# Optimization experiments

Hardware: AMD Instinct MI355X
Metric: run time of the kernel (lower is better)

The kernel has to match this reference:

```python
import jax, jax.numpy as jnp
import numpy as np

SIGNAL_LEN = 2048
N_WAVELETS = 32
TWO_PI = 2.0 * np.pi


def _encoder(x, W1, b1, W2, b2, W3, b3, W4, b4):
    B = x.shape[0]
    h = x.reshape(B, -1)                      # (B, 4096)
    h = jax.nn.relu(h @ W1.T + b1)            # (B, 1024)
    h = jax.nn.relu(h @ W2.T + b2)            # (B, 512)
    h = jax.nn.relu(h @ W3.T + b3)            # (B, 256)
    return h @ W4.T + b4                      # (B, n_wavelets*5)


def _synthesize(params):
    # params: (B, N_WAVELETS, 5)
    A = params[..., 0]                                    # (B, N)
    t0 = jax.nn.sigmoid(params[..., 1]) * SIGNAL_LEN      # (B, N)
    f = jax.nn.sigmoid(params[..., 2]) * 0.5              # (B, N)
    sigma = jax.nn.sigmoid(params[..., 3]) * 200.0 + 2.0  # (B, N)
    phi = params[..., 4]                                  # (B, N)

    t = jnp.arange(SIGNAL_LEN, dtype=params.dtype)        # (T,)
    dt = t[None, None, :] - t0[..., None]                 # (B, N, T)
    g = (A[..., None]
         * jnp.exp(-(dt * dt) / (2.0 * sigma[..., None] ** 2))
         * jnp.cos(TWO_PI * f[..., None] * dt + phi[..., None]))  # (B, N, T)
    sig = jnp.sum(g, axis=1)                              # (B, T)
    # both channels receive the identical wavelet sum (as in the torch code)
    return jnp.stack([sig, sig], axis=1)                  # (B, 2, T)


def setup_inputs() -> dict:
    key = jax.random.key(0)
    ks = jax.random.split(key, 9)
    B = 4096
    def w(k, shape, fan_in):
        return jax.random.normal(k, shape, dtype=jnp.float32) / np.sqrt(fan_in)
    return {
        "x": jax.random.normal(ks[0], (B, 2, SIGNAL_LEN), dtype=jnp.float32),
        "W1": w(ks[1], (1024, 4096), 4096), "b1": jnp.zeros((1024,), jnp.float32),
        "W2": w(ks[2], (512, 1024), 1024),  "b2": jnp.zeros((512,), jnp.float32),
        "W3": w(ks[3], (256, 512), 512),    "b3": jnp.zeros((256,), jnp.float32),
        "W4": w(ks[4], (N_WAVELETS * 5, 256), 256), "b4": jnp.zeros((N_WAVELETS * 5,), jnp.float32),
    }


def reference(x, W1, b1, W2, b2, W3, b3, W4, b4):
    B = x.shape[0]
    params = _encoder(x, W1, b1, W2, b2, W3, b3, W4, b4).reshape(B, N_WAVELETS, 5)
    return _synthesize(params)  # (B, 2, SIGNAL_LEN)
```

## Files before the change

### kernel.cpp

```cpp
#include <hip/hip_runtime.h>


#define SIGNAL_LEN 2048
#define NWAV 32

typedef _Float16 f16x8 __attribute__((ext_vector_type(8)));
typedef _Float16 f16x4 __attribute__((ext_vector_type(4)));
typedef float    f32x4 __attribute__((ext_vector_type(4)));

__device__ __forceinline__ void load16_lds(const _Float16* g, _Float16* l) {
  __builtin_amdgcn_global_load_lds((const __attribute__((address_space(1))) void*)g,
                                   (__attribute__((address_space(3))) void*)l,
                                   16, 0, 0);
}

struct HL { _Float16 h, l; };
__device__ __forceinline__ HL split_one(float a) {
  HL r;
  r.h = (_Float16)a;
  r.l = (_Float16)((a - (float)r.h) * 4096.0f);
  return r;
}

__global__ void split_x(const float4* __restrict__ src, f16x4* __restrict__ dh,
                        f16x4* __restrict__ dl) {
  int i = blockIdx.x * 256 + threadIdx.x;
  float4 v = src[i];
  float a[4] = {v.x, v.y, v.z, v.w};
  f16x4 h, l;
#pragma unroll
  for (int j = 0; j < 4; j++) {
    HL r = split_one(a[j]);
    h[j] = r.h;
    l[j] = r.l;
  }
  dh[i] = h;
  dl[i] = l;
}

__global__ void split_weights(const float* __restrict__ W1, const float* __restrict__ W2,
                              const float* __restrict__ W3, const float* __restrict__ W4,
                              const float* __restrict__ b4,
                              f16x4* __restrict__ W1h, f16x4* __restrict__ W1l,
                              f16x4* __restrict__ W2h, f16x4* __restrict__ W2l,
                              f16x4* __restrict__ W3h, f16x4* __restrict__ W3l,
                              f16x4* __restrict__ W4h, f16x4* __restrict__ W4l,
                              float* __restrict__ b4p) {
  const int blk = blockIdx.x;
  const int tid = threadIdx.x;
  if (blk < 4736) {
    const float4* src;
    f16x4 *dh, *dl;
    int i;
    if (blk < 4096) {
      src = (const float4*)W1; dh = W1h; dl = W1l; i = blk * 256 + tid;
    } else if (blk < 4608) {
      src = (const float4*)W2; dh = W2h; dl = W2l; i = (blk - 4096) * 256 + tid;
    } else {
      src = (const float4*)W3; dh = W3h; dl = W3l; i = (blk - 4608) * 256 + tid;
    }
    float4 v = src[i];
    float a[4] = {v.x * 256.0f, v.y * 256.0f, v.z * 256.0f, v.w * 256.0f};
    f16x4 h, l;
#pragma unroll
    for (int j = 0; j < 4; j++) {
      HL r = split_one(a[j]);
      h[j] = r.h;
      l[j] = r.l;
    }
    dh[i] = h;
    dl[i] = l;
  } else if (blk < 4800) {
    int i = (blk - 4736) * 256 + tid;
    int i4 = i << 2;
    int row = i4 >> 8;
    f16x4 h, l;
#pragma unroll
    for (int j = 0; j < 4; j++) {
      float a = (row < 160) ? W4[i4 + j] * 256.0f : 0.0f;
      HL r = split_one(a);
      h[j] = r.h;
      l[j] = r.l;
    }
    W4h[i] = h;
    W4l[i] = l;
  } else {
    b4p[tid] = (tid < 160) ? b4[tid] : 0.0f;
  }
}

template <int TM, int TN, int N, int K, bool RELU, bool SPLIT_OUT>
__global__ void __launch_bounds__(256, 2)
gemm_db(const _Float16* __restrict__ Ah, const _Float16* __restrict__ Al,
        const _Float16* __restrict__ Bh, const _Float16* __restrict__ Bl,
        const float* __restrict__ bias,
        _Float16* __restrict__ Ch, _Float16* __restrict__ Cl,
        float* __restrict__ Cf) {
  constexpr int AM = TM / 32;
  constexpr int BN = TN / 32;
  constexpr int AU = TM / 8;
  constexpr int TU = (TM + TN) / 8;
  constexpr int UPW = TU / 4;
  constexpr int NK = K / 32;

  __shared__ __align__(16) _Float16 s[2][(TM + TN) * 64];

  const int tid = threadIdx.x;
  const int lane = tid & 63;
  const int w = tid >> 6;
  const int wm = w >> 1, wn = w & 1;
  const int m0 = blockIdx.y * TM;
  const int n0 = blockIdx.x * TN;

  const int srow = lane >> 2;
  const int sk8 = (((lane & 3) - (lane >> 3)) & 3) * 8;

  const _Float16* gb[UPW];
  int lo[UPW];
#pragma unroll
  for (int i = 0; i < UPW; ++i) {
    const int u = w * UPW + i;
    if (u < AU) {
      const int g = u >> 1, hl = u & 1;
      gb[i] = (hl ? Al : Ah) + (size_t)(m0 + g * 16 + srow) * K + sk8;
    } else {
      const int ub = u - AU;
      const int g = ub >> 1, hl = ub & 1;
      gb[i] = (hl ? Bl : Bh) + (size_t)(n0 + g * 16 + srow) * K + sk8;
    }
    lo[i] = u * 512;
  }

  const int fr = lane & 15;
  const int fq = lane >> 4;
  const int fslot8 = (4 * fr + ((fq + (fr >> 1)) & 3)) * 8;

  f32x4 acc1[AM][BN], acc2[AM][BN];
#pragma unroll
  for (int i = 0; i < AM; i++)
#pragma unroll
    for (int j = 0; j < BN; j++) {
      acc1[i][j] = 0.0f;
      acc2[i][j] = 0.0f;
    }

#pragma unroll
  for (int i = 0; i < UPW; ++i) load16_lds(gb[i], &s[0][lo[i]]);

  for (int kt = 0; kt < NK; ++kt) {
    const int cur = kt & 1;
    __syncthreads();

    if (kt + 1 < NK) {
      const int kofs = (kt + 1) * 32;
#pragma unroll
      for (int i = 0; i < UPW; ++i) load16_lds(gb[i] + kofs, &s[cur ^ 1][lo[i]]);
    }

    f16x8 fAh[AM], fAl[AM], fBh[BN], fBl[BN];
#pragma unroll
    for (int im = 0; im < AM; ++im) {
      const int g = wm * AM + im;
      fAh[im] = *(const f16x8*)(&s[cur][(g * 2 + 0) * 512 + fslot8]);
      fAl[im] = *(const f16x8*)(&s[cur][(g * 2 + 1) * 512 + fslot8]);
    }
#pragma unroll
    for (int in = 0; in < BN; ++in) {
      const int g = wn * BN + in;
      fBh[in] = *(const f16x8*)(&s[cur][TM * 64 + (g * 2 + 0) * 512 + fslot8]);
      fBl[in] = *(const f16x8*)(&s[cur][TM * 64 + (g * 2 + 1) * 512 + fslot8]);
    }
#pragma unroll
    for (int im = 0; im < AM; ++im) {
#pragma unroll
      for (int in = 0; in < BN; ++in) {
        acc1[im][in] = __builtin_amdgcn_mfma_f32_16x16x32_f16(fAh[im], fBh[in], acc1[im][in], 0, 0, 0);
        acc2[im][in] = __builtin_amdgcn_mfma_f32_16x16x32_f16(fAh[im], fBl[in], acc2[im][in], 0, 0, 0);
        acc2[im][in] = __builtin_amdgcn_mfma_f32_16x16x32_f16(fAl[im], fBh[in], acc2[im][in], 0, 0, 0);
      }
    }
  }

  const int quad = lane >> 4;
#pragma unroll
  for (int in = 0; in < BN; ++in) {
    const int n = n0 + wn * (TN / 2) + in * 16 + fr;
    const float bv = bias[n];
#pragma unroll
    for (int im = 0; im < AM; ++im) {
#pragma unroll
      for (int r = 0; r < 4; ++r) {
        const int m = m0 + wm * (TM / 2) + im * 16 + quad * 4 + r;
        float c = (acc1[im][in][r] + acc2[im][in][r] * (1.0f / 4096.0f)) * (1.0f / 256.0f) + bv;
        if (RELU) c = fmaxf(c, 0.0f);
        const size_t off = (size_t)m * N + n;
        if (SPLIT_OUT) {
          HL rr = split_one(c);
          Ch[off] = rr.h;
          Cl[off] = rr.l;
        } else {
          Cf[off] = c;
        }
      }
    }
  }
}

__global__ void __launch_bounds__(256)
synth(const float* __restrict__ P, float* __restrict__ out) {
  __shared__ float sA[NWAV], sT0[NWAV], sF[NWAV], sC[NWAV], sPh[NWAV], sSg[NWAV];
  const int b = blockIdx.x;
  const int tid = threadIdx.x;
  if (tid < NWAV) {
    const float* q = P + (size_t)b * 256 + tid * 5;
    const float L2E = 1.44269504088896340736f;
    float A = q[0], p1 = q[1], p2 = q[2], p3 = q[3], p4 = q[4];
    float s1 = 1.0f / (1.0f + exp2f(-p1 * L2E));
    float s2 = 1.0f / (1.0f + exp2f(-p2 * L2E));
    float s3 = 1.0f / (1.0f + exp2f(-p3 * L2E));
    float sg = s3 * 200.0f + 2.0f;
    sA[tid] = A;
    sT0[tid] = s1 * 2048.0f;
    sF[tid] = s2 * 0.5f;
    sC[tid] = -L2E / (2.0f * sg * sg);
    sPh[tid] = p4 * 0.15915494309189535f;
    sSg[tid] = sg;
  }
  __syncthreads();

  const float t0f = (float)(tid * 8);
  const int wlo = (tid & ~63) * 8;
  float acc[8];
#pragma unroll
  for (int i = 0; i < 8; i++) acc[i] = 0.0f;

  for (int wv = 0; wv < NWAV; wv++) {
    const float t0 = sT0[wv], sg = sSg[wv];
    if (t0 + 5.0f * sg < (float)wlo || t0 - 5.0f * sg > (float)(wlo + 511)) continue;
    const float A = sA[wv], fr = sF[wv], cn = sC[wv], ph = sPh[wv];
#pragma unroll
    for (int i = 0; i < 8; i++) {
      float dt = (t0f + (float)i) - t0;
      float e = exp2f(dt * dt * cn);
      float r = fr * dt + ph;
      r -= floorf(r);
      float cs = __builtin_amdgcn_cosf(r);
      acc[i] += A * e * cs;
    }
  }

  float* o = out + (size_t)b * (2 * SIGNAL_LEN) + tid * 8;
  float4 v0 = make_float4(acc[0], acc[1], acc[2], acc[3]);
  float4 v1 = make_float4(acc[4], acc[5], acc[6], acc[7]);
  *(float4*)(o) = v0;
  *(float4*)(o + 4) = v1;
  *(float4*)(o + SIGNAL_LEN) = v0;
  *(float4*)(o + SIGNAL_LEN + 4) = v1;
}

extern "C" void kernel_launch(void* const* d_in, const int* in_sizes, int n_in,
                              void* d_out, int out_size, void* d_ws, size_t ws_size,
                              hipStream_t stream) {
  (void)in_sizes; (void)n_in; (void)out_size; (void)ws_size;
  const float* X  = (const float*)d_in[0];
  const float* W1 = (const float*)d_in[1];
  const float* b1 = (const float*)d_in[2];
  const float* W2 = (const float*)d_in[3];
  const float* b2 = (const float*)d_in[4];
  const float* W3 = (const float*)d_in[5];
  const float* b3 = (const float*)d_in[6];
  const float* W4 = (const float*)d_in[7];
  const float* b4 = (const float*)d_in[8];
  float* out = (float*)d_out;

  char* p = (char*)d_ws;
  auto take = [&](size_t bytes) -> char* {
    char* r = p;
    p += (bytes + 255) & ~(size_t)255;
    return r;
  };
  _Float16* Xh  = (_Float16*)take((size_t)4096 * 4096 * 2);
  _Float16* Xl  = (_Float16*)take((size_t)4096 * 4096 * 2);
  _Float16* W1h = (_Float16*)take((size_t)1024 * 4096 * 2);
  _Float16* W1l = (_Float16*)take((size_t)1024 * 4096 * 2);
  _Float16* H1h = (_Float16*)take((size_t)4096 * 1024 * 2);
  _Float16* H1l = (_Float16*)take((size_t)4096 * 1024 * 2);
  _Float16* W2h = (_Float16*)take((size_t)512 * 1024 * 2);
  _Float16* W2l = (_Float16*)take((size_t)512 * 1024 * 2);
  _Float16* H2h = (_Float16*)take((size_t)4096 * 512 * 2);
  _Float16* H2l = (_Float16*)take((size_t)4096 * 512 * 2);
  _Float16* W3h = (_Float16*)take((size_t)256 * 512 * 2);
  _Float16* W3l = (_Float16*)take((size_t)256 * 512 * 2);
  _Float16* H3h = (_Float16*)take((size_t)4096 * 256 * 2);
  _Float16* H3l = (_Float16*)take((size_t)4096 * 256 * 2);
  _Float16* W4h = (_Float16*)take((size_t)256 * 256 * 2);
  _Float16* W4l = (_Float16*)take((size_t)256 * 256 * 2);
  float*    b4p = (float*)take(256 * 4);
  float*    Pp  = (float*)take((size_t)4096 * 256 * 4);

  split_x<<<16384, 256, 0, stream>>>((const float4*)X, (f16x4*)Xh, (f16x4*)Xl);
  split_weights<<<4801, 256, 0, stream>>>(W1, W2, W3, W4, b4,
                                          (f16x4*)W1h, (f16x4*)W1l, (f16x4*)W2h, (f16x4*)W2l,
                                          (f16x4*)W3h, (f16x4*)W3l, (f16x4*)W4h, (f16x4*)W4l, b4p);

  gemm_db<128, 128, 1024, 4096, true, true><<<dim3(8, 32), 256, 0, stream>>>(
      Xh, Xl, W1h, W1l, b1, H1h, H1l, nullptr);
  gemm_db<64, 128, 512, 1024, true, true><<<dim3(4, 64), 256, 0, stream>>>(
      H1h, H1l, W2h, W2l, b2, H2h, H2l, nullptr);
  gemm_db<64, 64, 256, 512, true, true><<<dim3(4, 64), 256, 0, stream>>>(
      H2h, H2l, W3h, W3l, b3, H3h, H3l, nullptr);
  gemm_db<64, 64, 256, 256, false, false><<<dim3(4, 64), 256, 0, stream>>>(
      H3h, H3l, W4h, W4l, b4p, nullptr, nullptr, Pp);

  synth<<<4096, 256, 0, stream>>>(Pp, out);
}
```

Before: 405.4 us.

## Split GEMM K dimension in two and add a separate combine epilogue kernel

Each encoder GEMM now runs with a two-way split over K via a grid z-dimension. Each split writes fp32 partial sums to a scratch buffer, and a new combine kernel adds them, applies scale, bias and ReLU, and re-splits the result into fp16 hi/lo pairs. The aim is to double the block count so more of the GPU's compute units are busy, since the first GEMM had only 256 blocks. The cost is extra fp32 partial-sum traffic through global memory and four additional kernel launches.

Measured after the change: 437.4 us. 1.08x slower.

```diff
diff --git a/kernel.cpp b/kernel.cpp
--- a/kernel.cpp
+++ b/kernel.cpp
@@ -89,19 +89,17 @@
   }
 }
 
-template <int TM, int TN, int N, int K, bool RELU, bool SPLIT_OUT>
+template <int TM, int TN, int N, int K, int KSPLIT>
 __global__ void __launch_bounds__(256, 2)
 gemm_db(const _Float16* __restrict__ Ah, const _Float16* __restrict__ Al,
         const _Float16* __restrict__ Bh, const _Float16* __restrict__ Bl,
-        const float* __restrict__ bias,
-        _Float16* __restrict__ Ch, _Float16* __restrict__ Cl,
-        float* __restrict__ Cf) {
+        float* __restrict__ Cp) {
   constexpr int AM = TM / 32;
   constexpr int BN = TN / 32;
   constexpr int AU = TM / 8;
   constexpr int TU = (TM + TN) / 8;
   constexpr int UPW = TU / 4;
-  constexpr int NK = K / 32;
+  constexpr int NK = K / KSPLIT / 32;
 
   __shared__ __align__(16) _Float16 s[2][(TM + TN) * 64];
 
@@ -111,6 +109,7 @@
   const int wm = w >> 1, wn = w & 1;
   const int m0 = blockIdx.y * TM;
   const int n0 = blockIdx.x * TN;
+  const int kb = blockIdx.z * (K / KSPLIT);
 
   const int srow = lane >> 2;
   const int sk8 = (((lane & 3) - (lane >> 3)) & 3) * 8;
@@ -122,11 +121,11 @@
     const int u = w * UPW + i;
     if (u < AU) {
       const int g = u >> 1, hl = u & 1;
-      gb[i] = (hl ? Al : Ah) + (size_t)(m0 + g * 16 + srow) * K + sk8;
+      gb[i] = (hl ? Al : Ah) + (size_t)(m0 + g * 16 + srow) * K + kb + sk8;
     } else {
       const int ub = u - AU;
       const int g = ub >> 1, hl = ub & 1;
-      gb[i] = (hl ? Bl : Bh) + (size_t)(n0 + g * 16 + srow) * K + sk8;
+      gb[i] = (hl ? Bl : Bh) + (size_t)(n0 + g * 16 + srow) * K + kb + sk8;
     }
     lo[i] = u * 512;
   }
@@ -182,27 +181,50 @@
   }
 
   const int quad = lane >> 4;
+  float* Cz = Cp + (size_t)blockIdx.z * ((size_t)gridDim.y * TM) * N;
 #pragma unroll
   for (int in = 0; in < BN; ++in) {
     const int n = n0 + wn * (TN / 2) + in * 16 + fr;
-    const float bv = bias[n];
 #pragma unroll
     for (int im = 0; im < AM; ++im) {
 #pragma unroll
       for (int r = 0; r < 4; ++r) {
         const int m = m0 + wm * (TM / 2) + im * 16 + quad * 4 + r;
-        float c = (acc1[im][in][r] + acc2[im][in][r] * (1.0f / 4096.0f)) * (1.0f / 256.0f) + bv;
-        if (RELU) c = fmaxf(c, 0.0f);
-        const size_t off = (size_t)m * N + n;
-        if (SPLIT_OUT) {
-          HL rr = split_one(c);
-          Ch[off] = rr.h;
-          Cl[off] = rr.l;
-        } else {
-          Cf[off] = c;
-        }
+        Cz[(size_t)m * N + n] = acc1[im][in][r] + acc2[im][in][r] * (1.0f / 4096.0f);
       }
     }
+  }
+}
+
+template <bool RELU, bool SPLIT_OUT>
+__global__ void __launch_bounds__(256)
+combine(const float* __restrict__ Cp, const float* __restrict__ bias, int N,
+        size_t halfN, _Float16* __restrict__ Ch, _Float16* __restrict__ Cl,
+        float* __restrict__ Cf) {
+  const size_t i4 = ((size_t)blockIdx.x * 256 + threadIdx.x) * 4;
+  float4 p0 = *(const float4*)(Cp + i4);
+  float4 p1 = *(const float4*)(Cp + halfN + i4);
+  float4 bv = *(const float4*)(bias + (i4 % (size_t)N));
+  float c[4] = {(p0.x + p1.x) * (1.0f / 256.0f) + bv.x,
+                (p0.y + p1.y) * (1.0f / 256.0f) + bv.y,
+                (p0.z + p1.z) * (1.0f / 256.0f) + bv.z,
+                (p0.w + p1.w) * (1.0f / 256.0f) + bv.w};
+  if (RELU) {
+#pragma unroll
+    for (int j = 0; j < 4; j++) c[j] = fmaxf(c[j], 0.0f);
+  }
+  if (SPLIT_OUT) {
+    f16x4 h, l;
+#pragma unroll
+    for (int j = 0; j < 4; j++) {
+      HL r = split_one(c[j]);
+      h[j] = r.h;
+      l[j] = r.l;
+    }
+    *(f16x4*)(Ch + i4) = h;
+    *(f16x4*)(Cl + i4) = l;
+  } else {
+    *(float4*)(Cf + i4) = make_float4(c[0], c[1], c[2], c[3]);
   }
 }
 
@@ -297,20 +319,32 @@
   _Float16* W4l = (_Float16*)take((size_t)256 * 256 * 2);
   float*    b4p = (float*)take(256 * 4);
   float*    Pp  = (float*)take((size_t)4096 * 256 * 4);
+  float*    Cp  = (float*)take((size_t)2 * 4096 * 1024 * 4);
 
   split_x<<<16384, 256, 0, stream>>>((const float4*)X, (f16x4*)Xh, (f16x4*)Xl);
   split_weights<<<4801, 256, 0, stream>>>(W1, W2, W3, W4, b4,
                                           (f16x4*)W1h, (f16x4*)W1l, (f16x4*)W2h, (f16x4*)W2l,
                                           (f16x4*)W3h, (f16x4*)W3l, (f16x4*)W4h, (f16x4*)W4l, b4p);
 
-  gemm_db<128, 128, 1024, 4096, true, true><<<dim3(8, 32), 256, 0, stream>>>(
-      Xh, Xl, W1h, W1l, b1, H1h, H1l, nullptr);
-  gemm_db<64, 128, 512, 1024, true, true><<<dim3(4, 64), 256, 0, stream>>>(
-      H1h, H1l, W2h, W2l, b2, H2h, H2l, nullptr);
-  gemm_db<64, 64, 256, 512, true, true><<<dim3(4, 64), 256, 0, stream>>>(
-      H2h, H2l, W3h, W3l, b3, H3h, H3l, nullptr);
-  gemm_db<64, 64, 256, 256, false, false><<<dim3(4, 64), 256, 0, stream>>>(
-      H3h, H3l, W4h, W4l, b4p, nullptr, nullptr, Pp);
+  gemm_db<128, 128, 1024, 4096, 2><<<dim3(8, 32, 2), 256, 0, stream>>>(
+      Xh, Xl, W1h, W1l, Cp);
+  combine<true, true><<<4096, 256, 0, stream>>>(
+      Cp, b1, 1024, (size_t)4096 * 1024, H1h, H1l, nullptr);
+
+  gemm_db<64, 128, 512, 1024, 2><<<dim3(4, 64, 2), 256, 0, stream>>>(
+      H1h, H1l, W2h, W2l, Cp);
+  combine<true, true><<<2048, 256, 0, stream>>>(
+      Cp, b2, 512, (size_t)4096 * 512, H2h, H2l, nullptr);
+
+  gemm_db<64, 64, 256, 512, 2><<<dim3(4, 64, 2), 256, 0, stream>>>(
+      H2h, H2l, W3h, W3l, Cp);
+  combine<true, true><<<1024, 256, 0, stream>>>(
+      Cp, b3, 256, (size_t)4096 * 256, H3h, H3l, nullptr);
+
+  gemm_db<64, 64, 256, 256, 2><<<dim3(4, 64, 2), 256, 0, stream>>>(
+      H3h, H3l, W4h, W4l, Cp);
+  combine<false, false><<<1024, 256, 0, stream>>>(
+      Cp, b4p, 256, (size_t)4096 * 256, nullptr, nullptr, Pp);
 
   synth<<<4096, 256, 0, stream>>>(Pp, out);
 }
```

## Split-K the first GEMM with larger tiles and a separate combine kernel

Applied to the files above, without the earlier changes.

The first layer GEMM (4096x1024x4096) changes from 128x128 tiles on a 256-block grid to 128x256 tiles split over K in two halves, still 256 blocks but with occupancy hint 1. Each half writes fp32 partial sums to a new 32 MB buffer, and a combine kernel adds them, applies bias and ReLU, and splits the result into fp16 hi/lo. The larger N tile is meant to raise operand reuse per block. The cost is an extra fp32 round-trip of the partials, one more launch, and more registers per thread.

After: 404.3 us. Within noise of the previous version (-0.3%).

```diff
diff --git a/kernel.cpp b/kernel.cpp
--- a/kernel.cpp
+++ b/kernel.cpp
@@ -91,11 +91,11 @@
 
 template <int TM, int TN, int N, int K, bool RELU, bool SPLIT_OUT>
 __global__ void __launch_bounds__(256, 2)
-gemm_db(const _Float16* __restrict__ Ah, const _Float16* __restrict__ Al,
-        const _Float16* __restrict__ Bh, const _Float16* __restrict__ Bl,
-        const float* __restrict__ bias,
-        _Float16* __restrict__ Ch, _Float16* __restrict__ Cl,
-        float* __restrict__ Cf) {
+gemm_fused(const _Float16* __restrict__ Ah, const _Float16* __restrict__ Al,
+           const _Float16* __restrict__ Bh, const _Float16* __restrict__ Bl,
+           const float* __restrict__ bias,
+           _Float16* __restrict__ Ch, _Float16* __restrict__ Cl,
+           float* __restrict__ Cf) {
   constexpr int AM = TM / 32;
   constexpr int BN = TN / 32;
   constexpr int AU = TM / 8;
@@ -204,6 +204,136 @@
       }
     }
   }
+}
+
+template <int TM, int TN, int N, int K, int KSPLIT, int MINW>
+__global__ void __launch_bounds__(256, MINW)
+gemm_part(const _Float16* __restrict__ Ah, const _Float16* __restrict__ Al,
+          const _Float16* __restrict__ Bh, const _Float16* __restrict__ Bl,
+          float* __restrict__ Cp) {
+  constexpr int AM = TM / 32;
+  constexpr int BN = TN / 32;
+  constexpr int AU = TM / 8;
+  constexpr int TU = (TM + TN) / 8;
+  constexpr int UPW = TU / 4;
+  constexpr int NK = K / KSPLIT / 32;
+
+  __shared__ __align__(16) _Float16 s[2][(TM + TN) * 64];
+
+  const int tid = threadIdx.x;
+  const int lane = tid & 63;
+  const int w = tid >> 6;
+  const int wm = w >> 1, wn = w & 1;
+  const int m0 = blockIdx.y * TM;
+  const int n0 = blockIdx.x * TN;
+  const int kb = blockIdx.z * (K / KSPLIT);
+
+  const int srow = lane >> 2;
+  const int sk8 = (((lane & 3) - (lane >> 3)) & 3) * 8;
+
+  const _Float16* gb[UPW];
+  int lo[UPW];
+#pragma unroll
+  for (int i = 0; i < UPW; ++i) {
+    const int u = w * UPW + i;
+    if (u < AU) {
+      const int g = u >> 1, hl = u & 1;
+      gb[i] = (hl ? Al : Ah) + (size_t)(m0 + g * 16 + srow) * K + kb + sk8;
+    } else {
+      const int ub = u - AU;
+      const int g = ub >> 1, hl = ub & 1;
+      gb[i] = (hl ? Bl : Bh) + (size_t)(n0 + g * 16 + srow) * K + kb + sk8;
+    }
+    lo[i] = u * 512;
+  }
+
+  const int fr = lane & 15;
+  const int fq = lane >> 4;
+  const int fslot8 = (4 * fr + ((fq + (fr >> 1)) & 3)) * 8;
+
+  f32x4 acc1[AM][BN], acc2[AM][BN];
+#pragma unroll
+  for (int i = 0; i < AM; i++)
+#pragma unroll
+    for (int j = 0; j < BN; j++) {
+      acc1[i][j] = 0.0f;
+      acc2[i][j] = 0.0f;
+    }
+
+#pragma unroll
+  for (int i = 0; i < UPW; ++i) load16_lds(gb[i], &s[0][lo[i]]);
+
+  for (int kt = 0; kt < NK; ++kt) {
+    const int cur = kt & 1;
+    __syncthreads();
+
+    if (kt + 1 < NK) {
+      const int kofs = (kt + 1) * 32;
+#pragma unroll
+      for (int i = 0; i < UPW; ++i) load16_lds(gb[i] + kofs, &s[cur ^ 1][lo[i]]);
+    }
+
+    f16x8 fAh[AM], fAl[AM], fBh[BN], fBl[BN];
+#pragma unroll
+    for (int im = 0; im < AM; ++im) {
+      const int g = wm * AM + im;
+      fAh[im] = *(const f16x8*)(&s[cur][(g * 2 + 0) * 512 + fslot8]);
+      fAl[im] = *(const f16x8*)(&s[cur][(g * 2 + 1) * 512 + fslot8]);
+    }
+#pragma unroll
+    for (int in = 0; in < BN; ++in) {
+      const int g = wn * BN + in;
+      fBh[in] = *(const f16x8*)(&s[cur][TM * 64 + (g * 2 + 0) * 512 + fslot8]);
+      fBl[in] = *(const f16x8*)(&s[cur][TM * 64 + (g * 2 + 1) * 512 + fslot8]);
+    }
+#pragma unroll
+    for (int im = 0; im < AM; ++im) {
+#pragma unroll
+      for (int in = 0; in < BN; ++in) {
+        acc1[im][in] = __builtin_amdgcn_mfma_f32_16x16x32_f16(fAh[im], fBh[in], acc1[im][in], 0, 0, 0);
+        acc2[im][in] = __builtin_amdgcn_mfma_f32_16x16x32_f16(fAh[im], fBl[in], acc2[im][in], 0, 0, 0);
+        acc2[im][in] = __builtin_amdgcn_mfma_f32_16x16x32_f16(fAl[im], fBh[in], acc2[im][in], 0, 0, 0);
+      }
+    }
+  }
+
+  const int quad = lane >> 4;
+  float* Cz = Cp + (size_t)blockIdx.z * ((size_t)gridDim.y * TM) * N;
+#pragma unroll
+  for (int in = 0; in < BN; ++in) {
+    const int n = n0 + wn * (TN / 2) + in * 16 + fr;
+#pragma unroll
+    for (int im = 0; im < AM; ++im) {
+#pragma unroll
+      for (int r = 0; r < 4; ++r) {
+        const int m = m0 + wm * (TM / 2) + im * 16 + quad * 4 + r;
+        Cz[(size_t)m * N + n] = acc1[im][in][r] + acc2[im][in][r] * (1.0f / 4096.0f);
+      }
+    }
+  }
+}
+
+__global__ void __launch_bounds__(256)
+combine1(const float* __restrict__ Cp, const float* __restrict__ bias, int N,
+         size_t halfN, _Float16* __restrict__ Ch, _Float16* __restrict__ Cl) {
+  const size_t i4 = ((size_t)blockIdx.x * 256 + threadIdx.x) * 4;
+  float4 p0 = *(const float4*)(Cp + i4);
+  float4 p1 = *(const float4*)(Cp + halfN + i4);
+  float4 bv = *(const float4*)(bias + (i4 % (size_t)N));
+  float c[4] = {(p0.x + p1.x) * (1.0f / 256.0f) + bv.x,
+                (p0.y + p1.y) * (1.0f / 256.0f) + bv.y,
+                (p0.z + p1.z) * (1.0f / 256.0f) + bv.z,
+                (p0.w + p1.w) * (1.0f / 256.0f) + bv.w};
+  f16x4 h, l;
+#pragma unroll
+  for (int j = 0; j < 4; j++) {
+    c[j] = fmaxf(c[j], 0.0f);
+    HL r = split_one(c[j]);
+    h[j] = r.h;
+    l[j] = r.l;
+  }
+  *(f16x4*)(Ch + i4) = h;
+  *(f16x4*)(Cl + i4) = l;
 }
 
 __global__ void __launch_bounds__(256)
@@ -297,19 +427,22 @@
   _Float16* W4l = (_Float16*)take((size_t)256 * 256 * 2);
   float*    b4p = (float*)take(256 * 4);
   float*    Pp  = (float*)take((size_t)4096 * 256 * 4);
+  float*    Cp  = (float*)take((size_t)2 * 4096 * 1024 * 4);
 
   split_x<<<16384, 256, 0, stream>>>((const float4*)X, (f16x4*)Xh, (f16x4*)Xl);
   split_weights<<<4801, 256, 0, stream>>>(W1, W2, W3, W4, b4,
                                           (f16x4*)W1h, (f16x4*)W1l, (f16x4*)W2h, (f16x4*)W2l,
                                           (f16x4*)W3h, (f16x4*)W3l, (f16x4*)W4h, (f16x4*)W4l, b4p);
 
-  gemm_db<128, 128, 1024, 4096, true, true><<<dim3(8, 32), 256, 0, stream>>>(
-      Xh, Xl, W1h, W1l, b1, H1h, H1l, nullptr);
-  gemm_db<64, 128, 512, 1024, true, true><<<dim3(4, 64), 256, 0, stream>>>(
+  gemm_part<128, 256, 1024, 4096, 2, 1><<<dim3(4, 32, 2), 256, 0, stream>>>(
+      Xh, Xl, W1h, W1l, Cp);
+  combine1<<<4096, 256, 0, stream>>>(Cp, b1, 1024, (size_t)4096 * 1024, H1h, H1l);
+
+  gemm_fused<64, 128, 512, 1024, true, true><<<dim3(4, 64), 256, 0, stream>>>(
       H1h, H1l, W2h, W2l, b2, H2h, H2l, nullptr);
-  gemm_db<64, 64, 256, 512, true, true><<<dim3(4, 64), 256, 0, stream>>>(
+  gemm_fused<64, 64, 256, 512, true, true><<<dim3(4, 64), 256, 0, stream>>>(
       H2h, H2l, W3h, W3l, b3, H3h, H3l, nullptr);
-  gemm_db<64, 64, 256, 256, false, false><<<dim3(4, 64), 256, 0, stream>>>(
+  gemm_fused<64, 64, 256, 256, false, false><<<dim3(4, 64), 256, 0, stream>>>(
       H3h, H3l, W4h, W4l, b4p, nullptr, nullptr, Pp);
 
   synth<<<4096, 256, 0, stream>>>(Pp, out);
```
